# Kernel optimization log

Measured on AMD Instinct MI355X. Metric: run time of the kernel, lower is better.

Reference implementation:

```python
import jax, jax.numpy as jnp
import numpy as np
import math

EPS = 1e-8
LN_EPS = 1e-5
B, S, E, NH = 2, 2048, 1024, 4
DH = E // NH


def setup_inputs() -> dict:
    key = jax.random.key(0)
    ks = jax.random.split(key, 7)
    std_g = math.sqrt(2.0 / (5.0 * 3 * E))
    return {
        "q": jax.random.normal(ks[0], (B, S, E), dtype=jnp.float32),
        "k": jax.random.normal(ks[1], (B, S, E), dtype=jnp.float32),
        "v": jax.random.normal(ks[2], (B, S, E), dtype=jnp.float32),
        "igate_w": jax.random.normal(ks[3], (NH, 3 * E), dtype=jnp.float32) * std_g,
        "igate_b": jax.random.normal(ks[4], (NH,), dtype=jnp.float32) * 0.1,
        "fgate_w": jax.random.normal(ks[5], (NH, 3 * E), dtype=jnp.float32) * std_g,
        "fgate_b": jnp.linspace(3.4, 6.0, NH, dtype=jnp.float32),
        "out_w": jnp.zeros((E,), dtype=jnp.float32),  # residual affine weight (scale = 1 + out_w)
    }


def _mlstm_cell(q, k, v, igate_w, igate_b, fgate_w, fgate_b, out_w):
    Bq, Sq, Eq = q.shape
    # gate pre-activations from concatenated q,k,v: [B,S,NH]
    if_in = jnp.concatenate([q, k, v], axis=-1)
    ig = jnp.einsum("bsf,hf->bsh", if_in, igate_w) + igate_b
    fg = jnp.einsum("bsf,hf->bsh", if_in, fgate_w) + fgate_b
    ig = jnp.transpose(ig, (0, 2, 1))[..., None]  # [B,NH,S,1]
    fg = jnp.transpose(fg, (0, 2, 1))[..., None]  # [B,NH,S,1]

    # split heads: [B,NH,S,DH]
    qh = q.reshape(Bq, Sq, NH, DH).transpose(0, 2, 1, 3)
    kh = k.reshape(Bq, Sq, NH, DH).transpose(0, 2, 1, 3)
    vh = v.reshape(Bq, Sq, NH, DH).transpose(0, 2, 1, 3)

    # cumulative log forget gates -> causal decay matrix (log space)
    log_fg = jax.nn.log_sigmoid(fg)                           # [B,NH,S,1]
    cs = jnp.cumsum(log_fg, axis=2)                           # [B,NH,S,1]
    cs_shift = jnp.concatenate([jnp.zeros_like(cs[:, :, :1]), cs[:, :, :-1]], axis=2)
    # log_fg_matrix[i,j] = cumsum[i] - cumsum[j-1], masked causal
    logfg_mat = cs - jnp.swapaxes(cs_shift, -2, -1)           # [B,NH,S,S]
    ltr = jnp.tril(jnp.ones((Sq, Sq), dtype=bool))
    logfg_mat = jnp.where(ltr, logfg_mat, -jnp.inf)
    log_D = logfg_mat + jnp.swapaxes(ig, -2, -1)              # + igate row broadcast [B,NH,1,S]

    max_log_D = jnp.max(log_D, axis=-1, keepdims=True)        # [B,NH,S,1]
    D = jnp.exp(log_D - max_log_D)                            # stabilized decay matrix

    qk = jnp.einsum("bhsd,bhtd->bhst", qh, kh / math.sqrt(DH))
    C = qk * D
    sum_C_abs = jnp.abs(jnp.sum(C, axis=-1, keepdims=True))
    normaliser = jnp.maximum(sum_C_abs, jnp.exp(-max_log_D))  # robust normalizer
    C_norm = C / (normaliser + EPS)
    h = jnp.einsum("bhst,bhtd->bhsd", C_norm, vh)             # [B,NH,S,DH]

    # MultiHeadLayerNorm == group_norm with NH groups, per-channel residual weight
    mean = jnp.mean(h, axis=-1, keepdims=True)
    var = jnp.mean((h - mean) ** 2, axis=-1, keepdims=True)
    h_norm = (h - mean) / jnp.sqrt(var + LN_EPS)
    scale = (1.0 + out_w).reshape(1, NH, 1, DH)
    h_norm = h_norm * scale

    return h_norm.transpose(0, 2, 1, 3).reshape(Bq, Sq, Eq)


def reference(q, k, v, igate_w, igate_b, fgate_w, fgate_b, out_w):
    return _mlstm_cell(q, k, v, igate_w, igate_b, fgate_w, fgate_b, out_w)
```

## Files before the change

### kernel.cpp

```cpp
#include <hip/hip_runtime.h>
#include <hip/hip_bf16.h>
#include <math.h>

#define Bb  2
#define Ss  2048
#define Ee  1024
#define NHh 4
#define DHh 256
#define BH  (Bb*NHh)
#define TI  64
#define TIB 128
#define TJ  32
#define NT2 (Ss/TI)
#define NJT (Ss/TJ)

typedef short        s8v   __attribute__((ext_vector_type(8)));
typedef float        f4v   __attribute__((ext_vector_type(4)));
typedef float        f16v  __attribute__((ext_vector_type(16)));
typedef unsigned int u4v   __attribute__((ext_vector_type(4)));
typedef unsigned int u2v   __attribute__((ext_vector_type(2)));

__device__ inline unsigned pkbf2(float a, float b) {
    __hip_bfloat162 h2 = __float22bfloat162_rn(float2{a, b});
    unsigned u;
    __builtin_memcpy(&u, &h2, 4);
    return u;
}

__device__ inline void async16(const void* g, void* l) {
    __builtin_amdgcn_global_load_lds(
        (const __attribute__((address_space(1))) void*)g,
        (__attribute__((address_space(3))) void*)l, 16, 0, 0);
}

__global__ __launch_bounds__(256) void gates_prep_kernel(
    const float* __restrict__ q, const float* __restrict__ k, const float* __restrict__ v,
    const float* __restrict__ igw, const float* __restrict__ igb,
    const float* __restrict__ fgw, const float* __restrict__ fgb,
    float* __restrict__ ig_out, float* __restrict__ fg_out,
    unsigned short* __restrict__ Kimg, unsigned short* __restrict__ Vimg)
{
    int bidx = blockIdx.x;
    int tid = threadIdx.x;

    if (bidx >= 512) {
        int pidx = bidx - 512;
        int bh = pidx >> 6, jt = pidx & 63;
        int b = bh >> 2, h = bh & 3;
        int J0 = jt * TJ;
        const size_t hoff = (size_t)h * DHh;
        unsigned short* Kt = Kimg + (size_t)pidx * 1024 * 8;
        unsigned short* Vt = Vimg + (size_t)pidx * 1024 * 8;

        {
            int kR = tid >> 3, kc0 = tid & 7;
            const float* src = k + ((size_t)(b * Ss + J0 + kR)) * Ee + hoff;
#pragma unroll
            for (int p = 0; p < 4; p++) {
                int cc = kc0 + 8 * p;
                float4 x0 = ((const float4*)(src + cc * 8))[0];
                float4 x1 = ((const float4*)(src + cc * 8))[1];
                u4v wv;
                wv.x = pkbf2(x0.x, x0.y); wv.y = pkbf2(x0.z, x0.w);
                wv.z = pkbf2(x1.x, x1.y); wv.w = pkbf2(x1.z, x1.w);
                *(u4v*)&Kt[(kR * 32 + (cc ^ (kR & 7))) * 8] = wv;
            }
        }
        {
            int vdp = tid & 127, vjb = tid >> 7;
            int d0 = vdp * 2;
#pragma unroll
            for (int p = 0; p < 2; p++) {
                int jc = vjb + 2 * p;
                const float* vbase = v + ((size_t)(b * Ss + J0 + jc * 8)) * Ee + hoff + d0;
                float2 e0 = *(const float2*)(vbase);
                float2 e1 = *(const float2*)(vbase + Ee);
                float2 e2 = *(const float2*)(vbase + 2 * Ee);
                float2 e3 = *(const float2*)(vbase + 3 * Ee);
                float2 e4 = *(const float2*)(vbase + 4 * Ee);
                float2 e5 = *(const float2*)(vbase + 5 * Ee);
                float2 e6 = *(const float2*)(vbase + 6 * Ee);
                float2 e7 = *(const float2*)(vbase + 7 * Ee);
                int swz = jc ^ (vdp & 3);
                u4v w0, w1;
                w0.x = pkbf2(e0.x, e1.x); w0.y = pkbf2(e2.x, e3.x);
                w0.z = pkbf2(e4.x, e5.x); w0.w = pkbf2(e6.x, e7.x);
                w1.x = pkbf2(e0.y, e1.y); w1.y = pkbf2(e2.y, e3.y);
                w1.z = pkbf2(e4.y, e5.y); w1.w = pkbf2(e6.y, e7.y);
                *(u4v*)&Vt[(d0 * 4 + swz) * 8] = w0;
                *(u4v*)&Vt[((d0 + 1) * 4 + swz) * 8] = w1;
            }
        }
        return;
    }

    int sc = bidx >> 1, hp = bidx & 1;
    __shared__ float wl[4][3072];
    __shared__ float pw[4][8];

#pragma unroll
    for (int c = 0; c < 4; c++) {
        int h = hp * 2 + (c >> 1);
        const float* src = ((c & 1) ? fgw : igw) + (size_t)h * 3 * Ee;
        for (int idx = tid * 4; idx < 3 * Ee; idx += 1024)
            *(float4*)&wl[c][idx] = *(const float4*)(src + idx);
    }
    __syncthreads();

    int c4 = tid * 4;
    int w = tid >> 6, lane = tid & 63;

    for (int sp = 0; sp < 8; sp++) {
        int bs0 = sc * 16 + sp * 2;
        float4 qa = *(const float4*)(q + (size_t)bs0 * Ee + c4);
        float4 ka = *(const float4*)(k + (size_t)bs0 * Ee + c4);
        float4 va = *(const float4*)(v + (size_t)bs0 * Ee + c4);
        float4 qb = *(const float4*)(q + (size_t)(bs0 + 1) * Ee + c4);
        float4 kb = *(const float4*)(k + (size_t)(bs0 + 1) * Ee + c4);
        float4 vb = *(const float4*)(v + (size_t)(bs0 + 1) * Ee + c4);
        float red[8];
#pragma unroll
        for (int c = 0; c < 4; c++) {
            const float* wc = wl[c];
            float4 wq = *(const float4*)&wc[c4];
            float4 wk = *(const float4*)&wc[Ee + c4];
            float4 wv = *(const float4*)&wc[2 * Ee + c4];
            float x0 = qa.x*wq.x + qa.y*wq.y + qa.z*wq.z + qa.w*wq.w
                     + ka.x*wk.x + ka.y*wk.y + ka.z*wk.z + ka.w*wk.w
                     + va.x*wv.x + va.y*wv.y + va.z*wv.z + va.w*wv.w;
            float x1 = qb.x*wq.x + qb.y*wq.y + qb.z*wq.z + qb.w*wq.w
                     + kb.x*wk.x + kb.y*wk.y + kb.z*wk.z + kb.w*wk.w
                     + vb.x*wv.x + vb.y*wv.y + vb.z*wv.z + vb.w*wv.w;
            for (int off = 32; off > 0; off >>= 1) {
                x0 += __shfl_down(x0, off, 64);
                x1 += __shfl_down(x1, off, 64);
            }
            red[c] = x0; red[4 + c] = x1;
        }
        __syncthreads();
        if (lane == 0) {
#pragma unroll
            for (int c = 0; c < 8; c++) pw[w][c] = red[c];
        }
        __syncthreads();
        if (tid < 8) {
            float t = pw[0][tid] + pw[1][tid] + pw[2][tid] + pw[3][tid];
            int rr = tid >> 2, cc = tid & 3;
            int h = hp * 2 + (cc >> 1);
            int bs = bs0 + rr;
            int b = bs >> 11, s = bs & 2047;
            size_t o = ((size_t)(b * NHh + h)) * Ss + s;
            if (cc & 1) fg_out[o] = t + fgb[h];
            else        ig_out[o] = t + igb[h];
        }
    }
}

#define CHUNK 8
__global__ __launch_bounds__(256) void scan_kernel(
    const float* __restrict__ ig, const float* __restrict__ fg,
    float* __restrict__ a_out, float* __restrict__ M_out, float* __restrict__ nf_out)
{
    int bh = blockIdx.x;
    int tid = threadIdx.x;
    const float* igp = ig + (size_t)bh * Ss;
    const float* fgp = fg + (size_t)bh * Ss;
    int s0 = tid * CHUNK;

    float ls[CHUNK], cs[CHUNK];
    float tot = 0.f;
#pragma unroll
    for (int c = 0; c < CHUNK; c++) {
        float x = fgp[s0 + c];
        float l = fminf(x, 0.f) - log1pf(expf(-fabsf(x)));
        ls[c] = l; tot += l; cs[c] = tot;
    }
    __shared__ float sc[256];
    sc[tid] = tot; __syncthreads();
    for (int off = 1; off < 256; off <<= 1) {
        float add = (tid >= off) ? sc[tid - off] : 0.f;
        __syncthreads();
        sc[tid] += add;
        __syncthreads();
    }
    float excl = sc[tid] - tot;

    float av[CHUNK], pmax[CHUNK];
    float tmax = -INFINITY;
#pragma unroll
    for (int c = 0; c < CHUNK; c++) {
        float csf  = excl + cs[c];
        float csm1 = csf - ls[c];
        float a = igp[s0 + c] - csm1;
        av[c] = a;
        tmax = fmaxf(tmax, a);
        pmax[c] = tmax;
        cs[c] = csf;
    }
    __shared__ float sm[256];
    sm[tid] = tmax; __syncthreads();
    for (int off = 1; off < 256; off <<= 1) {
        float other = (tid >= off) ? sm[tid - off] : -INFINITY;
        __syncthreads();
        sm[tid] = fmaxf(sm[tid], other);
        __syncthreads();
    }
    float emax = (tid > 0) ? sm[tid - 1] : -INFINITY;
#pragma unroll
    for (int c = 0; c < CHUNK; c++) {
        float M = fmaxf(emax, pmax[c]);
        size_t o = (size_t)bh * Ss + s0 + c;
        a_out[o]  = av[c];
        M_out[o]  = M;
        nf_out[o] = expf(-cs[c] - M);
    }
}

__global__ __launch_bounds__(256, 3) void mlstm_ch(
    const float* __restrict__ qp,
    const unsigned short* __restrict__ Kimg, const unsigned short* __restrict__ Vimg,
    const float* __restrict__ a_ws, const float* __restrict__ M_ws,
    float* __restrict__ outF, float* __restrict__ Hpart, float* __restrict__ rsbuf)
{
    int bidx = blockIdx.x;
    int bh = bidx & 7;
    int c  = bidx >> 3;
    int b = bh >> 2, h = bh & 3;
    int tid = threadIdx.x;

    const size_t hoff = (size_t)h * DHh;
    const size_t HP = (size_t)Bb * Ss * Ee;

    __shared__ unsigned short KF[1024 * 8];
    __shared__ unsigned short VF[1024 * 8];
    __shared__ unsigned short PF[256 * 8];
    __shared__ float a_s[TJ];
    __shared__ float rs_s[TI];

    const int iq   = tid >> 6;
    const int lane = tid & 63;
    const int lm = lane & 15, q4 = lane >> 4;
    const float inv_sqrt_dh = 0.0625f;

    const unsigned short* Kb = Kimg + (size_t)(bh * NJT) * 1024 * 8;
    const unsigned short* Vb = Vimg + (size_t)(bh * NJT) * 1024 * 8;
    const float* a_base = a_ws + (size_t)bh * Ss;

    int g    = c * 11;
    int gend = g + 11;
    int T = (int)((sqrtf((float)(4 * g + 1)) - 1.f) * 0.5f);
    while (T * (T + 1) > g) T--;
    while ((T + 1) * (T + 2) <= g) T++;

    while (g < gend) {
        const int tstart = T * (T + 1);
        const int tend   = tstart + 2 * T + 2;
        const int jt_beg = g - tstart;
        const int pend   = (gend < tend) ? gend : tend;
        const int jt_end = pend - tstart;
        const int ord    = c - tstart / 11;
        const int I0     = T * TI;
        float* Hdst = (ord == 0) ? outF : (Hpart + (size_t)(ord - 1) * HP);

        s8v qf[8];
        {
            const float* qrow = qp + ((size_t)(b * Ss + I0 + iq * 16 + lm)) * Ee + hoff;
#pragma unroll
            for (int ks = 0; ks < 8; ks++) {
                const float4* p = (const float4*)(qrow + ks * 32 + q4 * 8);
                float4 x0 = p[0], x1 = p[1];
                union { s8v v; unsigned u[4]; } rr;
                rr.u[0] = pkbf2(x0.x, x0.y);
                rr.u[1] = pkbf2(x0.z, x0.w);
                rr.u[2] = pkbf2(x1.x, x1.y);
                rr.u[3] = pkbf2(x1.z, x1.w);
                qf[ks] = rr.v;
            }
        }
        const int  i_row = I0 + iq * 16 + lm;
        const float Mi = M_ws[(size_t)bh * Ss + i_row];

        f4v acc[16];
#pragma unroll
        for (int t = 0; t < 16; t++) { acc[t][0]=0.f; acc[t][1]=0.f; acc[t][2]=0.f; acc[t][3]=0.f; }
        float rs_acc = 0.f;

        {
            const unsigned short* Kt = Kb + (size_t)jt_beg * 1024 * 8;
#pragma unroll
            for (int p = 0; p < 4; p++) {
                int cbase = (iq * 4 + p) * 64;
                async16(Kt + (size_t)(cbase + lane) * 8, &KF[cbase * 8]);
            }
            if (lane < 2)
                async16(a_base + (size_t)jt_beg * TJ + iq * 8 + lane * 4, &a_s[iq * 8]);
        }
        __syncthreads();

        for (int jt = jt_beg; jt < jt_end; jt++) {
            {
                const unsigned short* Vt = Vb + (size_t)jt * 1024 * 8;
#pragma unroll
                for (int p = 0; p < 4; p++) {
                    int cbase = (iq * 4 + p) * 64;
                    async16(Vt + (size_t)(cbase + lane) * 8, &VF[cbase * 8]);
                }
            }
            const int J0 = jt * TJ;

            f4v c0 = {0.f, 0.f, 0.f, 0.f}, c1 = c0;
            __builtin_amdgcn_s_setprio(1);
#pragma unroll
            for (int ks = 0; ks < 8; ks++) {
                int swzk = ((ks * 4 + q4) ^ (lm & 7)) * 8;
                s8v af0 = *(const s8v*)&KF[(lm * 32) * 8 + swzk];
                s8v af1 = *(const s8v*)&KF[((16 + lm) * 32) * 8 + swzk];
                c0 = __builtin_amdgcn_mfma_f32_16x16x32_bf16(af0, qf[ks], c0, 0, 0, 0);
                c1 = __builtin_amdgcn_mfma_f32_16x16x32_bf16(af1, qf[ks], c1, 0, 0, 0);
            }
            __builtin_amdgcn_s_setprio(0);
            {
                float rsum = 0.f;
#pragma unroll
                for (int t = 0; t < 2; t++) {
                    const f4v cc = t ? c1 : c0;
                    const int jb = t * 16 + q4 * 4;
                    float p[4];
#pragma unroll
                    for (int rr = 0; rr < 4; rr++) {
                        int jg = J0 + jb + rr;
                        float pv = 0.f;
                        if (jg <= i_row) pv = cc[rr] * inv_sqrt_dh * __expf(a_s[jb + rr] - Mi);
                        p[rr] = pv; rsum += pv;
                    }
                    u2v pwv;
                    pwv.x = pkbf2(p[0], p[1]);
                    pwv.y = pkbf2(p[2], p[3]);
                    int kb = t * 2 + (q4 >> 1);
                    *(u2v*)&PF[(iq * 64 + lm * 4 + (kb ^ (lm & 3))) * 8 + (q4 & 1) * 4] = pwv;
                }
                rsum += __shfl_xor(rsum, 16);
                rsum += __shfl_xor(rsum, 32);
                rs_acc += rsum;
            }
            s8v pa = *(const s8v*)&PF[(iq * 64 + lm * 4 + (q4 ^ (lm & 3))) * 8];

            __syncthreads();

            if (jt + 1 < jt_end) {
                const unsigned short* Kt = Kb + (size_t)(jt + 1) * 1024 * 8;
#pragma unroll
                for (int p = 0; p < 4; p++) {
                    int cbase = (iq * 4 + p) * 64;
                    async16(Kt + (size_t)(cbase + lane) * 8, &KF[cbase * 8]);
                }
                if (lane < 2)
                    async16(a_base + (size_t)(jt + 1) * TJ + iq * 8 + lane * 4, &a_s[iq * 8]);
            }

            __builtin_amdgcn_s_setprio(1);
#pragma unroll
            for (int db = 0; db < 16; db++) {
                int d = db * 16 + lm;
                s8v vb = *(const s8v*)&VF[(d * 4 + (q4 ^ ((d >> 1) & 3))) * 8];
                acc[db] = __builtin_amdgcn_mfma_f32_16x16x32_bf16(pa, vb, acc[db], 0, 0, 0);
            }
            __builtin_amdgcn_s_setprio(0);

            __syncthreads();
        }

        if (q4 == 0) rs_s[iq * 16 + lm] = rs_acc;
        __syncthreads();
        if (tid < TI)
            rsbuf[(size_t)ord * BH * Ss + (size_t)bh * Ss + I0 + tid] = rs_s[tid];

#pragma unroll
        for (int rr = 0; rr < 4; rr++) {
            float* row = Hdst + ((size_t)(b * Ss + I0 + iq * 16 + q4 * 4 + rr)) * Ee + hoff + lm;
#pragma unroll
            for (int db = 0; db < 16; db++)
                row[db * 16] = acc[db][rr];
        }

        g = pend;
        if (g >= tend) T++;
    }
}

__global__ __launch_bounds__(256, 2) void mlstm_big2(
    const float* __restrict__ qp,
    const unsigned short* __restrict__ Kimg, const unsigned short* __restrict__ Vimg,
    const float* __restrict__ a_ws, const float* __restrict__ M_ws,
    float* __restrict__ outF, float* __restrict__ Hpart, float* __restrict__ rsbuf)
{
    int bidx = blockIdx.x;
    int qd = bidx >> 7, u = bidx & 127;
    int bh = u & 7;
    int r  = u >> 3;
    int T  = (qd < 2) ? (15 - r) : r;
    int sg = qd;
    int b = bh >> 2, h = bh & 3;
    int I0 = T * TIB;
    int tid = threadIdx.x;

    const int tot = 4 * T + 4;
    const int jt_beg = (sg * tot) / 4;
    const int jt_end = ((sg + 1) * tot) / 4;
    const size_t hoff = (size_t)h * DHh;
    float* Hdst = (sg == 0) ? outF : (Hpart + (size_t)(sg - 1) * Bb * Ss * Ee);

    __shared__ unsigned short KF[2][1024 * 8];
    __shared__ unsigned short VF[2][1024 * 8];
    __shared__ unsigned short PF[512 * 8];
    __shared__ float a_s[2][TJ];
    __shared__ float rs_s[TIB];

    const int iq   = tid >> 6;
    const int lane = tid & 63;
    const int lm = lane & 15, q4 = lane >> 4;

    s8v qf0[8], qf1[8];
    {
        const float* qrow0 = qp + ((size_t)(b * Ss + I0 + iq * 16 + lm)) * Ee + hoff;
        const float* qrow1 = qrow0 + (size_t)64 * Ee;
#pragma unroll
        for (int ks = 0; ks < 8; ks++) {
            const float4* p0 = (const float4*)(qrow0 + ks * 32 + q4 * 8);
            float4 x0 = p0[0], x1 = p0[1];
            union { s8v v; unsigned u[4]; } rr;
            rr.u[0] = pkbf2(x0.x, x0.y);
            rr.u[1] = pkbf2(x0.z, x0.w);
            rr.u[2] = pkbf2(x1.x, x1.y);
            rr.u[3] = pkbf2(x1.z, x1.w);
            qf0[ks] = rr.v;
            const float4* p1 = (const float4*)(qrow1 + ks * 32 + q4 * 8);
            float4 y0 = p1[0], y1 = p1[1];
            union { s8v v; unsigned u[4]; } ss;
            ss.u[0] = pkbf2(y0.x, y0.y);
            ss.u[1] = pkbf2(y0.z, y0.w);
            ss.u[2] = pkbf2(y1.x, y1.y);
            ss.u[3] = pkbf2(y1.z, y1.w);
            qf1[ks] = ss.v;
        }
    }
    const int  i_row0 = I0 + iq * 16 + lm;
    const int  i_row1 = i_row0 + 64;
    const float Mi0 = M_ws[(size_t)bh * Ss + i_row0];
    const float Mi1 = M_ws[(size_t)bh * Ss + i_row1];

    f4v acc0[16], acc1[16];
#pragma unroll
    for (int t = 0; t < 16; t++) {
        acc0[t][0]=0.f; acc0[t][1]=0.f; acc0[t][2]=0.f; acc0[t][3]=0.f;
        acc1[t][0]=0.f; acc1[t][1]=0.f; acc1[t][2]=0.f; acc1[t][3]=0.f;
    }
    float rs_a0 = 0.f, rs_a1 = 0.f;
    const float inv_sqrt_dh = 0.0625f;

    const unsigned short* Kb = Kimg + (size_t)(bh * NJT) * 1024 * 8;
    const unsigned short* Vb = Vimg + (size_t)(bh * NJT) * 1024 * 8;

    {
        const unsigned short* Kt = Kb + (size_t)jt_beg * 1024 * 8;
        const unsigned short* Vt = Vb + (size_t)jt_beg * 1024 * 8;
#pragma unroll
        for (int p = 0; p < 4; p++) {
            int cbase = (iq * 4 + p) * 64;
            async16(Kt + (size_t)(cbase + lane) * 8, &KF[0][cbase * 8]);
            async16(Vt + (size_t)(cbase + lane) * 8, &VF[0][cbase * 8]);
        }
        if (tid < TJ) a_s[0][tid] = a_ws[(size_t)bh * Ss + jt_beg * TJ + tid];
    }

    int cur = 0;
    for (int jt = jt_beg; jt < jt_end; jt++, cur ^= 1) {
        __syncthreads();

        if (jt + 1 < jt_end) {
            const unsigned short* Kt = Kb + (size_t)(jt + 1) * 1024 * 8;
            const unsigned short* Vt = Vb + (size_t)(jt + 1) * 1024 * 8;
#pragma unroll
            for (int p = 0; p < 4; p++) {
                int cbase = (iq * 4 + p) * 64;
                async16(Kt + (size_t)(cbase + lane) * 8, &KF[cur ^ 1][cbase * 8]);
                async16(Vt + (size_t)(cbase + lane) * 8, &VF[cur ^ 1][cbase * 8]);
            }
            if (tid < TJ) a_s[cur ^ 1][tid] = a_ws[(size_t)bh * Ss + (jt + 1) * TJ + tid];
        }
        const int J0 = jt * TJ;

        f4v c00 = {0.f,0.f,0.f,0.f}, c01 = c00, c10 = c00, c11 = c00;
#pragma unroll
        for (int ks = 0; ks < 8; ks++) {
            int swzk = ((ks * 4 + q4) ^ (lm & 7)) * 8;
            s8v af0 = *(const s8v*)&KF[cur][(lm * 32) * 8 + swzk];
            s8v af1 = *(const s8v*)&KF[cur][((16 + lm) * 32) * 8 + swzk];
            c00 = __builtin_amdgcn_mfma_f32_16x16x32_bf16(af0, qf0[ks], c00, 0, 0, 0);
            c01 = __builtin_amdgcn_mfma_f32_16x16x32_bf16(af1, qf0[ks], c01, 0, 0, 0);
            c10 = __builtin_amdgcn_mfma_f32_16x16x32_bf16(af0, qf1[ks], c10, 0, 0, 0);
            c11 = __builtin_amdgcn_mfma_f32_16x16x32_bf16(af1, qf1[ks], c11, 0, 0, 0);
        }
        {
            float rsum0 = 0.f, rsum1 = 0.f;
#pragma unroll
            for (int t = 0; t < 2; t++) {
                const f4v ca = t ? c01 : c00;
                const f4v cb = t ? c11 : c10;
                const int jb = t * 16 + q4 * 4;
                float p0[4], p1[4];
#pragma unroll
                for (int rr = 0; rr < 4; rr++) {
                    int jg = J0 + jb + rr;
                    float ev = __expf(a_s[cur][jb + rr] - Mi0) * inv_sqrt_dh;
                    float ev1 = __expf(a_s[cur][jb + rr] - Mi1) * inv_sqrt_dh;
                    float pv0 = 0.f, pv1 = 0.f;
                    if (jg <= i_row0) pv0 = ca[rr] * ev;
                    if (jg <= i_row1) pv1 = cb[rr] * ev1;
                    p0[rr] = pv0; rsum0 += pv0;
                    p1[rr] = pv1; rsum1 += pv1;
                }
                int kb = t * 2 + (q4 >> 1);
                int cidx = (iq * 64 + lm * 4 + (kb ^ (lm & 3))) * 8 + (q4 & 1) * 4;
                u2v pw0, pw1;
                pw0.x = pkbf2(p0[0], p0[1]); pw0.y = pkbf2(p0[2], p0[3]);
                pw1.x = pkbf2(p1[0], p1[1]); pw1.y = pkbf2(p1[2], p1[3]);
                *(u2v*)&PF[cidx]            = pw0;
                *(u2v*)&PF[256 * 8 + cidx]  = pw1;
            }
            rsum0 += __shfl_xor(rsum0, 16);
            rsum0 += __shfl_xor(rsum0, 32);
            rs_a0 += rsum0;
            rsum1 += __shfl_xor(rsum1, 16);
            rsum1 += __shfl_xor(rsum1, 32);
            rs_a1 += rsum1;
        }
        int pidx = (iq * 64 + lm * 4 + (q4 ^ (lm & 3))) * 8;
        s8v pa0 = *(const s8v*)&PF[pidx];
        s8v pa1 = *(const s8v*)&PF[256 * 8 + pidx];

#pragma unroll
        for (int db = 0; db < 16; db++) {
            int d = db * 16 + lm;
            s8v vb = *(const s8v*)&VF[cur][(d * 4 + (q4 ^ ((d >> 1) & 3))) * 8];
            acc0[db] = __builtin_amdgcn_mfma_f32_16x16x32_bf16(pa0, vb, acc0[db], 0, 0, 0);
            acc1[db] = __builtin_amdgcn_mfma_f32_16x16x32_bf16(pa1, vb, acc1[db], 0, 0, 0);
        }
    }

    if (q4 == 0) {
        rs_s[iq * 16 + lm] = rs_a0;
        rs_s[64 + iq * 16 + lm] = rs_a1;
    }
    __syncthreads();
    if (tid < TIB)
        rsbuf[(size_t)sg * BH * Ss + (size_t)bh * Ss + I0 + tid] = rs_s[tid];

#pragma unroll
    for (int rr = 0; rr < 4; rr++) {
        float* row0 = Hdst + ((size_t)(b * Ss + I0 + iq * 16 + q4 * 4 + rr)) * Ee + hoff + lm;
        float* row1 = row0 + (size_t)64 * Ee;
#pragma unroll
        for (int db = 0; db < 16; db++) {
            row0[db * 16] = acc0[db][rr];
            row1[db * 16] = acc1[db][rr];
        }
    }
}

template<int PARTS>
__global__ __launch_bounds__(256, 4) void mlstm_fallback(
    const float* __restrict__ qp, const float* __restrict__ kp, const float* __restrict__ vp,
    const float* __restrict__ a_ws, const float* __restrict__ M_ws,
    float* __restrict__ outF, float* __restrict__ Hpart, float* __restrict__ rsbuf)
{
    int bidx = blockIdx.x;
    int bh, T, sg;
    if (PARTS == 1) {
        bh = bidx & 7; T = (NT2 - 1) - (bidx >> 3); sg = 0;
    } else {
        int qd = bidx >> 8, u = bidx & 255;
        bh = u & 7;
        int r = u >> 3;
        T  = qd ? r : (31 - r);
        sg = r & 1;
    }
    int b = bh >> 2, h = bh & 3;
    int I0 = T * TI;
    int tid = threadIdx.x;

    const int tot = 2 * T + 2;
    const int jt_beg = (sg * tot) / PARTS;
    const int jt_end = ((sg + 1) * tot) / PARTS;
    const size_t hoff = (size_t)h * DHh;
    float* Hdst = (sg == 0) ? outF : (Hpart + (size_t)(sg - 1) * Bb * Ss * Ee);

    if (jt_beg >= jt_end) {
        float4 z = {0.f, 0.f, 0.f, 0.f};
        for (int t = tid; t < TI * 64; t += 256) {
            int r2 = t >> 6, c = t & 63;
            *(float4*)(Hdst + ((size_t)(b * Ss + I0 + r2)) * Ee + hoff + 4 * c) = z;
        }
        if (tid < TI) rsbuf[(size_t)sg * BH * Ss + (size_t)bh * Ss + I0 + tid] = 0.f;
        return;
    }

    __shared__ unsigned short KF[1024 * 8];
    __shared__ unsigned short VF[1024 * 8];
    __shared__ unsigned short PF[256 * 8];
    __shared__ float a_s[TJ];
    __shared__ float rs_s[TI];

    const int iq   = tid >> 6;
    const int lane = tid & 63;
    const int lm = lane & 15, q4 = lane >> 4;
    const int m5 = lane & 31, hl = lane >> 5;

    s8v qf[8];
    {
        const float* qrow = qp + ((size_t)(b * Ss + I0 + iq * 16 + lm)) * Ee + hoff;
#pragma unroll
        for (int ks = 0; ks < 8; ks++) {
            const float4* p = (const float4*)(qrow + ks * 32 + q4 * 8);
            float4 x0 = p[0], x1 = p[1];
            union { s8v v; unsigned u[4]; } rr;
            rr.u[0] = pkbf2(x0.x, x0.y);
            rr.u[1] = pkbf2(x0.z, x0.w);
            rr.u[2] = pkbf2(x1.x, x1.y);
            rr.u[3] = pkbf2(x1.z, x1.w);
            qf[ks] = rr.v;
        }
    }
    const int  i_row = I0 + iq * 16 + lm;
    const float Mi = M_ws[(size_t)bh * Ss + i_row];

    f16v acc[4];
#pragma unroll
    for (int t = 0; t < 4; t++)
#pragma unroll
        for (int i = 0; i < 16; i++) acc[t][i] = 0.f;
    float rs_acc = 0.f;

    const float inv_sqrt_dh = 0.0625f;
    const int kR  = tid >> 3, kc0 = tid & 7;
    const int vdp = tid & 127, vjb = tid >> 7;

    for (int jt = jt_beg; jt < jt_end; jt++) {
        const int J0 = jt * TJ;
        __syncthreads();
        {
            const float* src = kp + ((size_t)(b * Ss + J0 + kR)) * Ee + hoff;
#pragma unroll
            for (int p = 0; p < 4; p++) {
                int cc = kc0 + 8 * p;
                float4 x0 = ((const float4*)(src + cc * 8))[0];
                float4 x1 = ((const float4*)(src + cc * 8))[1];
                u4v wv;
                wv.x = pkbf2(x0.x, x0.y); wv.y = pkbf2(x0.z, x0.w);
                wv.z = pkbf2(x1.x, x1.y); wv.w = pkbf2(x1.z, x1.w);
                *(u4v*)&KF[(kR * 32 + (cc ^ (kR & 7))) * 8] = wv;
            }
            int d0 = vdp * 2;
#pragma unroll
            for (int p = 0; p < 2; p++) {
                int jc = vjb + 2 * p;
                const float* vbase = vp + ((size_t)(b * Ss + J0 + jc * 8)) * Ee + hoff + d0;
                float2 e0 = *(const float2*)(vbase);
                float2 e1 = *(const float2*)(vbase + Ee);
                float2 e2 = *(const float2*)(vbase + 2 * Ee);
                float2 e3 = *(const float2*)(vbase + 3 * Ee);
                float2 e4 = *(const float2*)(vbase + 4 * Ee);
                float2 e5 = *(const float2*)(vbase + 5 * Ee);
                float2 e6 = *(const float2*)(vbase + 6 * Ee);
                float2 e7 = *(const float2*)(vbase + 7 * Ee);
                int swz = jc ^ (vdp & 3);
                u4v w0, w1;
                w0.x = pkbf2(e0.x, e1.x); w0.y = pkbf2(e2.x, e3.x);
                w0.z = pkbf2(e4.x, e5.x); w0.w = pkbf2(e6.x, e7.x);
                w1.x = pkbf2(e0.y, e1.y); w1.y = pkbf2(e2.y, e3.y);
                w1.z = pkbf2(e4.y, e5.y); w1.w = pkbf2(e6.y, e7.y);
                *(u4v*)&VF[(d0 * 4 + swz) * 8] = w0;
                *(u4v*)&VF[((d0 + 1) * 4 + swz) * 8] = w1;
            }
        }
        if (tid < TJ) a_s[tid] = a_ws[(size_t)bh * Ss + J0 + tid];
        __syncthreads();

        f4v c0 = {0.f, 0.f, 0.f, 0.f}, c1 = c0;
#pragma unroll
        for (int ks = 0; ks < 8; ks++) {
            int swzk = ((ks * 4 + q4) ^ (lm & 7)) * 8;
            s8v af0 = *(const s8v*)&KF[(lm * 32) * 8 + swzk];
            s8v af1 = *(const s8v*)&KF[((16 + lm) * 32) * 8 + swzk];
            c0 = __builtin_amdgcn_mfma_f32_16x16x32_bf16(af0, qf[ks], c0, 0, 0, 0);
            c1 = __builtin_amdgcn_mfma_f32_16x16x32_bf16(af1, qf[ks], c1, 0, 0, 0);
        }
        {
            float rsum = 0.f;
#pragma unroll
            for (int t = 0; t < 2; t++) {
                const f4v cc = t ? c1 : c0;
                const int jb = t * 16 + q4 * 4;
                float p[4];
#pragma unroll
                for (int rr = 0; rr < 4; rr++) {
                    int jg = J0 + jb + rr;
                    float pv = 0.f;
                    if (jg <= i_row) pv = cc[rr] * inv_sqrt_dh * __expf(a_s[jb + rr] - Mi);
                    p[rr] = pv; rsum += pv;
                }
                u2v pwv;
                pwv.x = pkbf2(p[0], p[1]);
                pwv.y = pkbf2(p[2], p[3]);
                int i = iq * 16 + lm;
                int kb = t * 2 + (q4 >> 1);
                *(u2v*)&PF[(i * 4 + (kb ^ ((i >> 1) & 3))) * 8 + (q4 & 1) * 4] = pwv;
            }
            rsum += __shfl_xor(rsum, 16);
            rsum += __shfl_xor(rsum, 32);
            rs_acc += rsum;
        }
        __syncthreads();

#pragma unroll
        for (int ks2 = 0; ks2 < 2; ks2++) {
            int swz2 = ((ks2 * 2 + hl) ^ ((m5 >> 1) & 3)) * 8;
            s8v pa0 = *(const s8v*)&PF[(m5 * 4) * 8 + swz2];
            s8v pa1 = *(const s8v*)&PF[((32 + m5) * 4) * 8 + swz2];
            s8v vb0 = *(const s8v*)&VF[((iq * 32 + m5) * 4) * 8 + swz2];
            s8v vb1 = *(const s8v*)&VF[(((iq + 4) * 32 + m5) * 4) * 8 + swz2];
            acc[0] = __builtin_amdgcn_mfma_f32_32x32x16_bf16(pa0, vb0, acc[0], 0, 0, 0);
            acc[1] = __builtin_amdgcn_mfma_f32_32x32x16_bf16(pa0, vb1, acc[1], 0, 0, 0);
            acc[2] = __builtin_amdgcn_mfma_f32_32x32x16_bf16(pa1, vb0, acc[2], 0, 0, 0);
            acc[3] = __builtin_amdgcn_mfma_f32_32x32x16_bf16(pa1, vb1, acc[3], 0, 0, 0);
        }
    }

    if (q4 == 0) rs_s[iq * 16 + lm] = rs_acc;
    __syncthreads();
    if (tid < TI)
        rsbuf[(size_t)sg * BH * Ss + (size_t)bh * Ss + I0 + tid] = rs_s[tid];

#pragma unroll
    for (int im = 0; im < 2; im++)
#pragma unroll
        for (int ns = 0; ns < 2; ns++) {
            const f16v av = acc[im * 2 + ns];
            const int col = (iq + 4 * ns) * 32 + m5;
#pragma unroll
            for (int rr = 0; rr < 16; rr++) {
                int row = I0 + im * 32 + (rr & 3) + 8 * (rr >> 2) + 4 * hl;
                Hdst[((size_t)(b * Ss + row)) * Ee + hoff + col] = av[rr];
            }
        }
}

__global__ __launch_bounds__(256) void combine_ch(
    const float* __restrict__ Hb, const float* __restrict__ rsbuf,
    const float* __restrict__ nf_ws, const float* __restrict__ out_w,
    float* __restrict__ outF)
{
    int rid = blockIdx.x * 4 + (threadIdx.x >> 6);
    int lane = threadIdx.x & 63;
    int bh = rid >> 11, s = rid & 2047;
    int b = bh >> 2, h = bh & 3;
    int T = s >> 6;
    int tstart = T * (T + 1);
    int tend   = tstart + 2 * T + 2;
    int p = (tend - 1) / 11 - tstart / 11 + 1;

    size_t base = ((size_t)(b * Ss + s)) * Ee + (size_t)h * DHh + lane * 4;
    const size_t HP = (size_t)Bb * Ss * Ee;
    float4 ha = *(const float4*)(outF + base);
    float rs = rsbuf[(size_t)bh * Ss + s];
    for (int k = 1; k < p; k++) {
        float4 hb = *(const float4*)(Hb + (size_t)(k - 1) * HP + base);
        ha.x += hb.x; ha.y += hb.y; ha.z += hb.z; ha.w += hb.w;
        rs += rsbuf[(size_t)k * BH * Ss + (size_t)bh * Ss + s];
    }
    float nfv = nf_ws[(size_t)bh * Ss + s];
    float invn = 1.f / (fmaxf(fabsf(rs), nfv) + 1e-8f);
    float4 x;
    x.x = ha.x * invn; x.y = ha.y * invn; x.z = ha.z * invn; x.w = ha.w * invn;
    float sx = x.x + x.y + x.z + x.w;
    float sq = x.x*x.x + x.y*x.y + x.z*x.z + x.w*x.w;
#pragma unroll
    for (int off = 1; off < 64; off <<= 1) {
        sx += __shfl_xor(sx, off);
        sq += __shfl_xor(sq, off);
    }
    float mean = sx * (1.f / DHh);
    float var  = sq * (1.f / DHh) - mean * mean;
    float rstd = rsqrtf(var + 1e-5f);
    float4 w4 = *(const float4*)(out_w + (size_t)h * DHh + lane * 4);
    float4 o;
    o.x = (x.x - mean) * rstd * (1.f + w4.x);
    o.y = (x.y - mean) * rstd * (1.f + w4.y);
    o.z = (x.z - mean) * rstd * (1.f + w4.z);
    o.w = (x.w - mean) * rstd * (1.f + w4.w);
    *(float4*)(outF + base) = o;
}

template<int PARTS>
__global__ __launch_bounds__(256) void combine_kernel(
    const float* __restrict__ Hb, const float* __restrict__ rsbuf,
    const float* __restrict__ nf_ws, const float* __restrict__ out_w,
    float* __restrict__ outF)
{
    int rid = blockIdx.x * 4 + (threadIdx.x >> 6);
    int lane = threadIdx.x & 63;
    int bh = rid >> 11, s = rid & 2047;
    int b = bh >> 2, h = bh & 3;
    size_t base = ((size_t)(b * Ss + s)) * Ee + (size_t)h * DHh + lane * 4;
    float4 ha = *(const float4*)(outF + base);
    float rs = rsbuf[(size_t)bh * Ss + s];
#pragma unroll
    for (int k = 1; k < PARTS; k++) {
        float4 hb = *(const float4*)(Hb + (size_t)(k - 1) * Bb * Ss * Ee + base);
        ha.x += hb.x; ha.y += hb.y; ha.z += hb.z; ha.w += hb.w;
        rs += rsbuf[(size_t)k * BH * Ss + (size_t)bh * Ss + s];
    }
    float nfv = nf_ws[(size_t)bh * Ss + s];
    float invn = 1.f / (fmaxf(fabsf(rs), nfv) + 1e-8f);
    float4 x;
    x.x = ha.x * invn; x.y = ha.y * invn; x.z = ha.z * invn; x.w = ha.w * invn;
    float sx = x.x + x.y + x.z + x.w;
    float sq = x.x*x.x + x.y*x.y + x.z*x.z + x.w*x.w;
#pragma unroll
    for (int off = 1; off < 64; off <<= 1) {
        sx += __shfl_xor(sx, off);
        sq += __shfl_xor(sq, off);
    }
    float mean = sx * (1.f / DHh);
    float var  = sq * (1.f / DHh) - mean * mean;
    float rstd = rsqrtf(var + 1e-5f);
    float4 w4 = *(const float4*)(out_w + (size_t)h * DHh + lane * 4);
    float4 o;
    o.x = (x.x - mean) * rstd * (1.f + w4.x);
    o.y = (x.y - mean) * rstd * (1.f + w4.y);
    o.z = (x.z - mean) * rstd * (1.f + w4.z);
    o.w = (x.w - mean) * rstd * (1.f + w4.w);
    *(float4*)(outF + base) = o;
}

extern "C" void kernel_launch(void* const* d_in, const int* in_sizes, int n_in,
                              void* d_out, int out_size, void* d_ws, size_t ws_size,
                              hipStream_t stream) {
    const float* q   = (const float*)d_in[0];
    const float* k   = (const float*)d_in[1];
    const float* v   = (const float*)d_in[2];
    const float* igw = (const float*)d_in[3];
    const float* igb = (const float*)d_in[4];
    const float* fgw = (const float*)d_in[5];
    const float* fgb = (const float*)d_in[6];
    const float* ow  = (const float*)d_in[7];
    float* out = (float*)d_out;

    float* ws = (float*)d_ws;
    float* ig = ws;
    float* fg = ws + 16384;
    float* aa = ws + 32768;
    float* MM = ws + 49152;
    float* nf = ws + 65536;
    float* rsb = ws + 81920;
    const size_t base_f = 81920 + 131072;
    unsigned short* KimgP = (unsigned short*)(ws + base_f);
    const size_t img_u = (size_t)BH * NJT * 1024 * 8;
    unsigned short* VimgP = KimgP + img_u;
    float* HpartImg = (float*)(VimgP + img_u);
    float* HpartRaw = ws + base_f;
    const size_t HP = (size_t)Bb * Ss * Ee;

    const size_t need_ch = base_f * 4 + 2 * img_u * 2 + 6 * HP * 4;
    const size_t need4   = base_f * 4 + 2 * img_u * 2 + 3 * HP * 4;
    const size_t need2   = base_f * 4 + 1 * HP * 4;

    if (ws_size >= need_ch) {
        gates_prep_kernel<<<1024, 256, 0, stream>>>(q, k, v, igw, igb, fgw, fgb,
                                                    ig, fg, KimgP, VimgP);
        scan_kernel<<<BH, 256, 0, stream>>>(ig, fg, aa, MM, nf);
        mlstm_ch<<<768, 256, 0, stream>>>(q, KimgP, VimgP, aa, MM,
                                          out, HpartImg, rsb);
        combine_ch<<<BH * Ss / 4, 256, 0, stream>>>(HpartImg, rsb, nf, ow, out);
    } else if (ws_size >= need4) {
        gates_prep_kernel<<<1024, 256, 0, stream>>>(q, k, v, igw, igb, fgw, fgb,
                                                    ig, fg, KimgP, VimgP);
        scan_kernel<<<BH, 256, 0, stream>>>(ig, fg, aa, MM, nf);
        mlstm_big2<<<512, 256, 0, stream>>>(q, KimgP, VimgP, aa, MM,
                                            out, HpartImg, rsb);
        combine_kernel<4><<<BH * Ss / 4, 256, 0, stream>>>(HpartImg, rsb, nf, ow, out);
    } else if (ws_size >= need2) {
        gates_prep_kernel<<<512, 256, 0, stream>>>(q, k, v, igw, igb, fgw, fgb,
                                                   ig, fg, nullptr, nullptr);
        scan_kernel<<<BH, 256, 0, stream>>>(ig, fg, aa, MM, nf);
        mlstm_fallback<2><<<512, 256, 0, stream>>>(q, k, v, aa, MM, out, HpartRaw, rsb);
        combine_kernel<2><<<BH * Ss / 4, 256, 0, stream>>>(HpartRaw, rsb, nf, ow, out);
    } else {
        gates_prep_kernel<<<512, 256, 0, stream>>>(q, k, v, igw, igb, fgw, fgb,
                                                   ig, fg, nullptr, nullptr);
        scan_kernel<<<BH, 256, 0, stream>>>(ig, fg, aa, MM, nf);
        mlstm_fallback<1><<<256, 256, 0, stream>>>(q, k, v, aa, MM, out, HpartRaw, rsb);
        combine_kernel<1><<<BH * Ss / 4, 256, 0, stream>>>(HpartRaw, rsb, nf, ow, out);
    }
}
```

Measured before the change: 186.7 us.

## Restructure gate projection so each wavefront computes all heads over row pairs

The gate pre-activation part of the prep kernel is rewritten. Previously each block staged two heads' weights in shared memory and reduced across four waves with block barriers. Now each wavefront owns row pairs, reads all four heads' ig/fg weights straight from global (cache-resident) memory, accumulates 16 partials in registers and reduces with shuffles only. This removes the shared-memory staging, the __syncthreads and the duplicate reads of q/k/v across head-pair blocks, and shrinks the gate grid from 512 to 128 blocks, at the cost of more registers and repeated global weight loads.

```diff
diff --git a/kernel.cpp b/kernel.cpp
--- a/kernel.cpp
+++ b/kernel.cpp
@@ -43,8 +43,8 @@
     int bidx = blockIdx.x;
     int tid = threadIdx.x;
 
-    if (bidx >= 512) {
-        int pidx = bidx - 512;
+    if (bidx >= 128) {
+        int pidx = bidx - 128;
         int bh = pidx >> 6, jt = pidx & 63;
         int b = bh >> 2, h = bh & 3;
         int J0 = jt * TJ;
@@ -94,64 +94,49 @@
         return;
     }
 
-    int sc = bidx >> 1, hp = bidx & 1;
-    __shared__ float wl[4][3072];
-    __shared__ float pw[4][8];
-
-#pragma unroll
-    for (int c = 0; c < 4; c++) {
-        int h = hp * 2 + (c >> 1);
-        const float* src = ((c & 1) ? fgw : igw) + (size_t)h * 3 * Ee;
-        for (int idx = tid * 4; idx < 3 * Ee; idx += 1024)
-            *(float4*)&wl[c][idx] = *(const float4*)(src + idx);
-    }
-    __syncthreads();
-
-    int c4 = tid * 4;
-    int w = tid >> 6, lane = tid & 63;
-
-    for (int sp = 0; sp < 8; sp++) {
-        int bs0 = sc * 16 + sp * 2;
-        float4 qa = *(const float4*)(q + (size_t)bs0 * Ee + c4);
-        float4 ka = *(const float4*)(k + (size_t)bs0 * Ee + c4);
-        float4 va = *(const float4*)(v + (size_t)bs0 * Ee + c4);
-        float4 qb = *(const float4*)(q + (size_t)(bs0 + 1) * Ee + c4);
-        float4 kb = *(const float4*)(k + (size_t)(bs0 + 1) * Ee + c4);
-        float4 vb = *(const float4*)(v + (size_t)(bs0 + 1) * Ee + c4);
-        float red[8];
-#pragma unroll
-        for (int c = 0; c < 4; c++) {
-            const float* wc = wl[c];
-            float4 wq = *(const float4*)&wc[c4];
-            float4 wk = *(const float4*)&wc[Ee + c4];
-            float4 wv = *(const float4*)&wc[2 * Ee + c4];
-            float x0 = qa.x*wq.x + qa.y*wq.y + qa.z*wq.z + qa.w*wq.w
-                     + ka.x*wk.x + ka.y*wk.y + ka.z*wk.z + ka.w*wk.w
-                     + va.x*wv.x + va.y*wv.y + va.z*wv.z + va.w*wv.w;
-            float x1 = qb.x*wq.x + qb.y*wq.y + qb.z*wq.z + qb.w*wq.w
-                     + kb.x*wk.x + kb.y*wk.y + kb.z*wk.z + kb.w*wk.w
-                     + vb.x*wv.x + vb.y*wv.y + vb.z*wv.z + vb.w*wv.w;
-            for (int off = 32; off > 0; off >>= 1) {
-                x0 += __shfl_down(x0, off, 64);
-                x1 += __shfl_down(x1, off, 64);
-            }
-            red[c] = x0; red[4 + c] = x1;
-        }
-        __syncthreads();
+    int wv = tid >> 6, lane = tid & 63;
+#pragma unroll 1
+    for (int p = 0; p < 4; p++) {
+        int bs0 = ((bidx * 4 + wv) * 4 + p) * 2;
+        float acc[16];
+#pragma unroll
+        for (int i = 0; i < 16; i++) acc[i] = 0.f;
+
+#pragma unroll
+        for (int j = 0; j < 12; j++) {
+            const float* src = (j < 4) ? q : ((j < 8) ? k : v);
+            int eoff = (j & 3) * 256 + lane * 4;
+            int woff = j * 256 + lane * 4;
+            float4 x0 = *(const float4*)(src + (size_t)bs0 * Ee + eoff);
+            float4 x1 = *(const float4*)(src + (size_t)(bs0 + 1) * Ee + eoff);
+#pragma unroll
+            for (int h = 0; h < 4; h++) {
+                float4 wi = *(const float4*)(igw + (size_t)h * 3 * Ee + woff);
+                float4 wf = *(const float4*)(fgw + (size_t)h * 3 * Ee + woff);
+                acc[h * 2]     += x0.x*wi.x + x0.y*wi.y + x0.z*wi.z + x0.w*wi.w;
+                acc[h * 2 + 1] += x0.x*wf.x + x0.y*wf.y + x0.z*wf.z + x0.w*wf.w;
+                acc[8 + h * 2]     += x1.x*wi.x + x1.y*wi.y + x1.z*wi.z + x1.w*wi.w;
+                acc[8 + h * 2 + 1] += x1.x*wf.x + x1.y*wf.y + x1.z*wf.z + x1.w*wf.w;
+            }
+        }
+#pragma unroll
+        for (int i = 0; i < 16; i++)
+            for (int off = 32; off > 0; off >>= 1)
+                acc[i] += __shfl_down(acc[i], off, 64);
         if (lane == 0) {
 #pragma unroll
-            for (int c = 0; c < 8; c++) pw[w][c] = red[c];
-        }
-        __syncthreads();
-        if (tid < 8) {
-            float t = pw[0][tid] + pw[1][tid] + pw[2][tid] + pw[3][tid];
-            int rr = tid >> 2, cc = tid & 3;
-            int h = hp * 2 + (cc >> 1);
-            int bs = bs0 + rr;
-            int b = bs >> 11, s = bs & 2047;
-            size_t o = ((size_t)(b * NHh + h)) * Ss + s;
-            if (cc & 1) fg_out[o] = t + fgb[h];
-            else        ig_out[o] = t + igb[h];
+            for (int c = 0; c < 8; c++) {
+                int h = c >> 1;
+#pragma unroll
+                for (int r = 0; r < 2; r++) {
+                    int bs = bs0 + r;
+                    int b = bs >> 11, s = bs & 2047;
+                    size_t o = ((size_t)(b * NHh + h)) * Ss + s;
+                    float val = acc[r * 8 + c];
+                    if (c & 1) fg_out[o] = val + fgb[h];
+                    else       ig_out[o] = val + igb[h];
+                }
+            }
         }
     }
 }
@@ -876,27 +861,27 @@
     const size_t need2   = base_f * 4 + 1 * HP * 4;
 
     if (ws_size >= need_ch) {
-        gates_prep_kernel<<<1024, 256, 0, stream>>>(q, k, v, igw, igb, fgw, fgb,
-                                                    ig, fg, KimgP, VimgP);
+        gates_prep_kernel<<<640, 256, 0, stream>>>(q, k, v, igw, igb, fgw, fgb,
+                                                   ig, fg, KimgP, VimgP);
         scan_kernel<<<BH, 256, 0, stream>>>(ig, fg, aa, MM, nf);
         mlstm_ch<<<768, 256, 0, stream>>>(q, KimgP, VimgP, aa, MM,
                                           out, HpartImg, rsb);
         combine_ch<<<BH * Ss / 4, 256, 0, stream>>>(HpartImg, rsb, nf, ow, out);
     } else if (ws_size >= need4) {
-        gates_prep_kernel<<<1024, 256, 0, stream>>>(q, k, v, igw, igb, fgw, fgb,
-                                                    ig, fg, KimgP, VimgP);
+        gates_prep_kernel<<<640, 256, 0, stream>>>(q, k, v, igw, igb, fgw, fgb,
+                                                   ig, fg, KimgP, VimgP);
         scan_kernel<<<BH, 256, 0, stream>>>(ig, fg, aa, MM, nf);
         mlstm_big2<<<512, 256, 0, stream>>>(q, KimgP, VimgP, aa, MM,
                                             out, HpartImg, rsb);
         combine_kernel<4><<<BH * Ss / 4, 256, 0, stream>>>(HpartImg, rsb, nf, ow, out);
     } else if (ws_size >= need2) {
-        gates_prep_kernel<<<512, 256, 0, stream>>>(q, k, v, igw, igb, fgw, fgb,
+        gates_prep_kernel<<<128, 256, 0, stream>>>(q, k, v, igw, igb, fgw, fgb,
                                                    ig, fg, nullptr, nullptr);
         scan_kernel<<<BH, 256, 0, stream>>>(ig, fg, aa, MM, nf);
         mlstm_fallback<2><<<512, 256, 0, stream>>>(q, k, v, aa, MM, out, HpartRaw, rsb);
         combine_kernel<2><<<BH * Ss / 4, 256, 0, stream>>>(HpartRaw, rsb, nf, ow, out);
     } else {
-        gates_prep_kernel<<<512, 256, 0, stream>>>(q, k, v, igw, igb, fgw, fgb,
+        gates_prep_kernel<<<128, 256, 0, stream>>>(q, k, v, igw, igb, fgw, fgb,
                                                    ig, fg, nullptr, nullptr);
         scan_kernel<<<BH, 256, 0, stream>>>(ig, fg, aa, MM, nf);
         mlstm_fallback<1><<<256, 256, 0, stream>>>(q, k, v, aa, MM, out, HpartRaw, rsb);
```

After: 245.5 us. 1.31x slower.
